# Kernel tuning notes

Hardware: AMD Instinct MI355X
Metric: run time of the kernel (lower is better)

## Reference

```python
import jax, jax.numpy as jnp
import numpy as np

# Config: 4 sparse batch items, each with 2048 active voxels (uniform-length case
# of sparse full self-attention). channels=1024, heads=16, head_dim=64.
B_SEQ, L, H, D = 4, 2048, 16, 64
C = H * D  # 1024
N = B_SEQ * L  # 8192
EPS = 1e-12  # F.normalize eps


def setup_inputs() -> dict:
    key = jax.random.key(0)
    ks = jax.random.split(key, 6)
    s = 1.0 / np.sqrt(C)
    return {
        "x": jax.random.normal(ks[0], (N, C), dtype=jnp.float32),
        "W_qkv": jax.random.normal(ks[1], (C, 3 * C), dtype=jnp.float32) * s,
        "b_qkv": jnp.zeros((3 * C,), dtype=jnp.float32),
        "gamma_q": jnp.ones((H, D), dtype=jnp.float32),
        "gamma_k": jnp.ones((H, D), dtype=jnp.float32),
        "W_out": jax.random.normal(ks[2], (C, C), dtype=jnp.float32) * s,
        "b_out": jnp.zeros((C,), dtype=jnp.float32),
    }


def _qk_rms_norm(t, gamma):
    # SparseMultiHeadRMSNorm: L2-normalize last dim, scale by gamma[h,d] * sqrt(D)
    norm = jnp.maximum(jnp.linalg.norm(t, axis=-1, keepdims=True), EPS)
    return (t / norm) * gamma * (D ** 0.5)


def reference(x, W_qkv, b_qkv, gamma_q, gamma_k, W_out, b_out):
    qkv = x @ W_qkv + b_qkv                       # [N, 3C]
    qkv = qkv.reshape(B_SEQ, L, 3, H, D)          # fused pre-reshape
    q, k, v = qkv[:, :, 0], qkv[:, :, 1], qkv[:, :, 2]  # [B,L,H,D]
    q = _qk_rms_norm(q, gamma_q)
    k = _qk_rms_norm(k, gamma_k)
    # full scaled dot-product attention within each sparse batch item
    scores = jnp.einsum('blhd,bmhd->bhlm', q, k) / (D ** 0.5)
    attn = jax.nn.softmax(scores, axis=-1)
    h = jnp.einsum('bhlm,bmhd->blhd', attn, v)    # [B,L,H,D]
    h = h.reshape(N, C)
    return h @ W_out + b_out
```

## Files before the change

kernel.cpp:

```cpp
#include <hip/hip_runtime.h>

using u16 = unsigned short;

typedef float  f32x4  __attribute__((ext_vector_type(4)));
typedef float  f32x16 __attribute__((ext_vector_type(16)));
typedef __bf16 bf16x8 __attribute__((ext_vector_type(8)));
typedef short  s16x8  __attribute__((ext_vector_type(8)));

#define DEVI __device__ __forceinline__

constexpr int TOK = 8192;
constexpr int CIN = 1024;
constexpr int C3  = 3072;
constexpr int NH  = 16;
constexpr int HD  = 64;
constexpr int SL  = 2048;
constexpr int BH  = 64;

constexpr float LOG2E = 1.4426950408889634f;

DEVI u16 f2bf(float x) {
  unsigned u = __builtin_bit_cast(unsigned, x);
  u += 0x7FFFu + ((u >> 16) & 1u);
  return (u16)(u >> 16);
}

DEVI f32x4 mfma16(s16x8 a, s16x8 b, f32x4 c) {
  return __builtin_amdgcn_mfma_f32_16x16x32_bf16(
      __builtin_bit_cast(bf16x8, a), __builtin_bit_cast(bf16x8, b), c, 0, 0, 0);
}

DEVI f32x16 mfma32(s16x8 a, s16x8 b, f32x16 c) {
  return __builtin_amdgcn_mfma_f32_32x32x16_bf16(
      __builtin_bit_cast(bf16x8, a), __builtin_bit_cast(bf16x8, b), c, 0, 0, 0);
}

DEVI void gload_lds16(const void* g, void* l) {
  __builtin_amdgcn_global_load_lds(
      (const __attribute__((address_space(1))) unsigned int*)g,
      (__attribute__((address_space(3))) unsigned int*)l, 16, 0, 0);
}

DEVI unsigned cvtpk(float lo, float hi) {
  unsigned r;
  asm("v_cvt_pk_bf16_f32 %0, %1, %2" : "=v"(r) : "v"(lo), "v"(hi));
  return r;
}

DEVI void plswap(unsigned& a, unsigned& b) {
  asm("v_permlane32_swap_b32 %0, %1" : "+v"(a), "+v"(b));
}

__global__ __launch_bounds__(256) void k_cvt_x(const float* __restrict__ x,
                                               u16* __restrict__ xb) {
  const int total = TOK * CIN / 4;
  for (int i = blockIdx.x * 256 + threadIdx.x; i < total; i += gridDim.x * 256) {
    float4 v = ((const float4*)x)[i];
    ushort4 o;
    o.x = f2bf(v.x); o.y = f2bf(v.y); o.z = f2bf(v.z); o.w = f2bf(v.w);
    ((ushort4*)xb)[i] = o;
  }
}

__global__ __launch_bounds__(256) void k_transpose(const float* __restrict__ in,
                                                   u16* __restrict__ out,
                                                   int R, int C) {
  __shared__ u16 t[64][72];
  int rt = R >> 6;
  int tr = (blockIdx.x % rt) << 6;
  int tc = (blockIdx.x / rt) << 6;
  int tid = threadIdx.x;
#pragma unroll
  for (int k2 = 0; k2 < 16; k2++) {
    int idx = k2 * 256 + tid;
    int r = idx >> 6, c = idx & 63;
    t[r][c] = f2bf(in[(size_t)(tr + r) * C + tc + c]);
  }
  __syncthreads();
#pragma unroll
  for (int k2 = 0; k2 < 16; k2++) {
    int idx = k2 * 256 + tid;
    int r = idx >> 6, c = idx & 63;
    out[(size_t)(tc + r) * R + tr + c] = t[c][r];
  }
}

__global__ __launch_bounds__(256) void k_bound(const float* __restrict__ gq,
                                               const float* __restrict__ gk,
                                               float* __restrict__ bnd) {
  const int tid = threadIdx.x;
  const int h = tid >> 4, s = tid & 15;
  float mv = 0.f;
#pragma unroll
  for (int j = 0; j < 4; j++) {
    int d = s * 4 + j;
    mv = fmaxf(mv, fabsf(gq[h * 64 + d] * gk[h * 64 + d]));
  }
  mv = fmaxf(mv, __shfl_xor(mv, 1));
  mv = fmaxf(mv, __shfl_xor(mv, 2));
  mv = fmaxf(mv, __shfl_xor(mv, 4));
  mv = fmaxf(mv, __shfl_xor(mv, 8));
  if (s == 0) bnd[h] = 8.0f * LOG2E * mv;
}

#define STAGE6(BUF, KT)                                                  \
  { char* Ld = L + (BUF) * 49152;                                        \
    const size_t ko = (size_t)(KT) * 128;                                \
    gload_lds16(Ab + ko,          Ld + wb);                              \
    gload_lds16(Ab + ko + 131072, Ld + 8192 + wb);                       \
    gload_lds16(Ab + ko + 262144, Ld + 16384 + wb);                      \
    gload_lds16(Ab + ko + 393216, Ld + 24576 + wb);                      \
    gload_lds16(Bb + ko,          Ld + 32768 + wb);                      \
    gload_lds16(Bb + ko + 131072, Ld + 40960 + wb); }

#define KBODY(KT, DOSTAGE, VMSTR)                                        \
  {                                                                      \
    if (DOSTAGE) STAGE6(((KT) + 2) % 3, (KT) + 2)                        \
    asm volatile("s_waitcnt " VMSTR ::: "memory");                       \
    __builtin_amdgcn_s_barrier();                                        \
    const char* Lb = L + ((KT) % 3) * 49152;                             \
    s16x8 af[4][2], bfr[4][2];                                           \
    _Pragma("unroll")                                                    \
    for (int mf = 0; mf < 4; mf++) {                                     \
      af[mf][0] = *(const s16x8*)(Lb + aoff + mf * 2048 + cx0);          \
      af[mf][1] = *(const s16x8*)(Lb + aoff + mf * 2048 + (cx0 ^ 64));   \
    }                                                                    \
    _Pragma("unroll")                                                    \
    for (int nf = 0; nf < 4; nf++) {                                     \
      bfr[nf][0] = *(const s16x8*)(Lb + boff + nf * 2048 + cx0);         \
      bfr[nf][1] = *(const s16x8*)(Lb + boff + nf * 2048 + (cx0 ^ 64));  \
    }                                                                    \
    __builtin_amdgcn_s_setprio(1);                                       \
    _Pragma("unroll")                                                    \
    for (int ks = 0; ks < 2; ks++)                                       \
      _Pragma("unroll")                                                  \
      for (int mf = 0; mf < 4; mf++)                                     \
        _Pragma("unroll")                                                \
        for (int nf = 0; nf < 4; nf++)                                   \
          acc[mf][nf] = mfma16(af[mf][ks], bfr[nf][ks], acc[mf][nf]);    \
    __builtin_amdgcn_s_setprio(0);                                       \
    __builtin_amdgcn_s_barrier();                                        \
  }

DEVI void gemm_mainloop(const char* Ab, const char* Bb, char* L,
                        int wb, int aoff, int boff, int cx0,
                        f32x4 (&acc)[4][4]) {
  STAGE6(0, 0)
  STAGE6(1, 1)
#pragma unroll
  for (int kt = 0; kt < 14; ++kt) KBODY(kt, 1, "vmcnt(12)")
  KBODY(14, 0, "vmcnt(6)")
  KBODY(15, 0, "vmcnt(0)")
}

__global__ __launch_bounds__(512, 2) void k_gemm_qkv(
    const u16* __restrict__ A, const u16* __restrict__ Bt,
    const float* __restrict__ bias, const float* __restrict__ gq,
    const float* __restrict__ gk,
    u16* __restrict__ Qn, u16* __restrict__ Kn, u16* __restrict__ Vt) {
  __shared__ __align__(16) char Lsh[3][49152];
  int bid = blockIdx.x;
  bid = (bid & 7) * 96 + (bid >> 3);
  const int bm = (bid / 24) * 256, bn = (bid % 24) * 128;
  const int tid = threadIdx.x, lane = tid & 63, w = tid >> 6;
  const int l15 = lane & 15, g = lane >> 4;
  const int wr4 = w >> 1, wc2 = w & 1;

  const int rA  = tid >> 3;
  const int scb = ((tid & 7) << 4) ^ ((rA & 7) << 4);
  const char* Ab = (const char*)A + (size_t)(bm + rA) * 2048 + scb;
  const char* Bb = (const char*)Bt + (size_t)(bn + rA) * 2048 + scb;
  const int wb   = w << 10;
  const int aoff = (wr4 * 64 + l15) * 128;
  const int boff = 32768 + (wc2 * 64 + l15) * 128;
  const int cx0  = (g ^ (l15 & 7)) << 4;

  f32x4 acc[4][4];
#pragma unroll
  for (int i = 0; i < 4; i++)
#pragma unroll
    for (int j = 0; j < 4; j++) acc[i][j] = f32x4{0.f, 0.f, 0.f, 0.f};

  gemm_mainloop(Ab, Bb, (char*)Lsh, wb, aoff, boff, cx0, acc);

  const int c0 = bn + wc2 * 64;
  const int sec = c0 >> 10;
  const int head = (c0 & 1023) >> 6;
  float bv[4], gv[4];
#pragma unroll
  for (int nf = 0; nf < 4; nf++) {
    bv[nf] = bias[c0 + nf * 16 + l15];
    gv[nf] = 1.f;
    if (sec == 0) gv[nf] = gq[head * 64 + nf * 16 + l15];
    if (sec == 1) gv[nf] = gk[head * 64 + nf * 16 + l15];
  }
#pragma unroll
  for (int mf = 0; mf < 4; mf++) {
#pragma unroll
    for (int nf = 0; nf < 4; nf++)
#pragma unroll
      for (int r = 0; r < 4; r++) acc[mf][nf][r] += bv[nf];
    if (sec < 2) {
#pragma unroll
      for (int r = 0; r < 4; r++) {
        float ss = 0.f;
#pragma unroll
        for (int nf = 0; nf < 4; nf++) ss += acc[mf][nf][r] * acc[mf][nf][r];
        ss += __shfl_xor(ss, 1); ss += __shfl_xor(ss, 2);
        ss += __shfl_xor(ss, 4); ss += __shfl_xor(ss, 8);
        float nrm = fmaxf(sqrtf(ss), 1e-12f);
        float f = (sec == 0 ? LOG2E : 8.0f) / nrm;
#pragma unroll
        for (int nf = 0; nf < 4; nf++) acc[mf][nf][r] *= f;
      }
    }
    int rbase = bm + wr4 * 64 + mf * 16 + 4 * g;
#pragma unroll
    for (int r = 0; r < 4; r++) {
      int row = rbase + r;
      int b = row >> 11, tok = row & 2047;
      int bh = b * NH + head;
#pragma unroll
      for (int nf = 0; nf < 4; nf++) {
        int d = nf * 16 + l15;
        u16 val = f2bf(acc[mf][nf][r] * gv[nf]);
        if (sec == 0)      Qn[((size_t)bh * SL + tok) * HD + d] = val;
        else if (sec == 1) Kn[((size_t)bh * SL + tok) * HD + d] = val;
        else               Vt[((size_t)bh * HD + d) * SL + tok] = val;
      }
    }
  }
}

__global__ __launch_bounds__(512, 2) void k_gemm_out(
    const u16* __restrict__ A, const u16* __restrict__ Bt,
    const float* __restrict__ bias, float* __restrict__ out) {
  __shared__ __align__(16) char Lsh[3][49152];
  int bid = blockIdx.x;
  bid = (bid & 7) * 32 + (bid >> 3);
  const int bm = (bid / 8) * 256, bn = (bid % 8) * 128;
  const int tid = threadIdx.x, lane = tid & 63, w = tid >> 6;
  const int l15 = lane & 15, g = lane >> 4;
  const int wr4 = w >> 1, wc2 = w & 1;

  const int rA  = tid >> 3;
  const int scb = ((tid & 7) << 4) ^ ((rA & 7) << 4);
  const char* Ab = (const char*)A + (size_t)(bm + rA) * 2048 + scb;
  const char* Bb = (const char*)Bt + (size_t)(bn + rA) * 2048 + scb;
  const int wb   = w << 10;
  const int aoff = (wr4 * 64 + l15) * 128;
  const int boff = 32768 + (wc2 * 64 + l15) * 128;
  const int cx0  = (g ^ (l15 & 7)) << 4;

  f32x4 acc[4][4];
#pragma unroll
  for (int i = 0; i < 4; i++)
#pragma unroll
    for (int j = 0; j < 4; j++) acc[i][j] = f32x4{0.f, 0.f, 0.f, 0.f};

  gemm_mainloop(Ab, Bb, (char*)Lsh, wb, aoff, boff, cx0, acc);

  float bv[4];
#pragma unroll
  for (int nf = 0; nf < 4; nf++) bv[nf] = bias[bn + wc2 * 64 + nf * 16 + l15];
#pragma unroll
  for (int mf = 0; mf < 4; mf++)
#pragma unroll
    for (int r = 0; r < 4; r++) {
      int row = bm + wr4 * 64 + mf * 16 + 4 * g + r;
#pragma unroll
      for (int nf = 0; nf < 4; nf++)
        out[(size_t)row * CIN + bn + wc2 * 64 + nf * 16 + l15] =
            acc[mf][nf][r] + bv[nf];
    }
}

__global__ __launch_bounds__(512) void k_attn(const u16* __restrict__ Qn,
                                              const u16* __restrict__ Kn,
                                              const u16* __restrict__ Vt,
                                              const float* __restrict__ bnd,
                                              u16* __restrict__ hm) {
  __shared__ __align__(16) char KL[2][8192];
  __shared__ __align__(16) char VL[2][8192];
  const int bh = blockIdx.x & 63, qb = blockIdx.x >> 6;
  const int tid = threadIdx.x, w = tid >> 6, lane = tid & 63;
  const int l31 = lane & 31, h = lane >> 5;
  const int qr0 = qb * 256 + w * 32;
  const float negM = -bnd[bh & 15];

  const int sr  = tid >> 3;
  const int scb = ((tid & 7) << 4) ^ ((sr & 7) << 4);
  const char* kst = (const char*)(Kn + (size_t)bh * SL * HD) + (size_t)sr * 128 + scb;
  const char* vst = (const char*)(Vt + (size_t)bh * HD * SL) + (size_t)sr * 4096 + scb;
  char* kl0 = KL[0] + (w << 10);
  char* vl0 = VL[0] + (w << 10);
  char* kl1 = KL[1] + (w << 10);
  char* vl1 = VL[1] + (w << 10);

  const u16* Qb = Qn + ((size_t)bh * SL + qr0 + l31) * HD + 8 * h;
  s16x8 qf[4];
#pragma unroll
  for (int ks = 0; ks < 4; ks++) qf[ks] = *(const s16x8*)(Qb + ks * 16);

  const int lb = l31 * 128 + ((h << 4) ^ ((l31 & 7) << 4));

  f32x16 o0, o1;
#pragma unroll
  for (int i = 0; i < 16; i++) { o0[i] = 0.f; o1[i] = 0.f; }
  float lr = 0.f;

  gload_lds16(kst, kl0);
  gload_lds16(vst, vl0);
  __syncthreads();

  for (int it = 0; it < 32; ++it) {
    const char* KB = (it & 1) ? KL[1] : KL[0];
    const char* VB = (it & 1) ? VL[1] : VL[0];
    if (it < 31) {
      const size_t ko = (size_t)(it + 1) << 13;
      const size_t vo = (size_t)(it + 1) << 7;
      gload_lds16(kst + ko, (it & 1) ? kl0 : kl1);
      gload_lds16(vst + vo, (it & 1) ? vl0 : vl1);
    }

    f32x16 s0, s1;
#pragma unroll
    for (int i = 0; i < 16; i++) { s0[i] = negM; s1[i] = negM; }
    __builtin_amdgcn_s_setprio(1);
#pragma unroll
    for (int ks = 0; ks < 4; ks++) {
      const s16x8 ka  = *(const s16x8*)(KB + (lb ^ (ks << 5)));
      const s16x8 kb2 = *(const s16x8*)(KB + 4096 + (lb ^ (ks << 5)));
      s0 = mfma32(ka, qf[ks], s0);
      s1 = mfma32(kb2, qf[ks], s1);
    }
    __builtin_amdgcn_s_setprio(0);

#pragma unroll
    for (int i = 0; i < 16; i++) s0[i] = __builtin_amdgcn_exp2f(s0[i]);
#pragma unroll
    for (int i = 0; i < 16; i++) s1[i] = __builtin_amdgcn_exp2f(s1[i]);
    float sm8[8];
#pragma unroll
    for (int i = 0; i < 8; i++)
      sm8[i] = (s0[i] + s0[i + 8]) + (s1[i] + s1[i + 8]);
    lr += ((sm8[0] + sm8[1]) + (sm8[2] + sm8[3])) +
          ((sm8[4] + sm8[5]) + (sm8[6] + sm8[7]));

    union PBu { unsigned u[4]; s16x8 v; } pb;
#define MK_PB(SV, B)                              \
    {                                             \
      unsigned a0 = cvtpk(SV[B + 0], SV[B + 1]);  \
      unsigned c0 = cvtpk(SV[B + 4], SV[B + 5]);  \
      plswap(a0, c0);                             \
      unsigned a1 = cvtpk(SV[B + 2], SV[B + 3]);  \
      unsigned c1 = cvtpk(SV[B + 6], SV[B + 7]);  \
      plswap(a1, c1);                             \
      pb.u[0] = a0; pb.u[1] = a1; pb.u[2] = c0; pb.u[3] = c1; \
    }
#define PV_STEP(KS)                                            \
    {                                                          \
      const s16x8 va = *(const s16x8*)(VB + (lb ^ (KS << 5))); \
      const s16x8 vb = *(const s16x8*)(VB + 4096 + (lb ^ (KS << 5))); \
      __builtin_amdgcn_s_setprio(1);                           \
      o0 = mfma32(va, pb.v, o0);                               \
      o1 = mfma32(vb, pb.v, o1);                               \
      __builtin_amdgcn_s_setprio(0);                           \
    }
    MK_PB(s0, 0) PV_STEP(0)
    MK_PB(s0, 8) PV_STEP(1)
    MK_PB(s1, 0) PV_STEP(2)
    MK_PB(s1, 8) PV_STEP(3)
#undef MK_PB
#undef PV_STEP

    __syncthreads();
  }

  const float ltot = lr + __shfl_xor(lr, 32);
  const float inv = 1.f / ltot;
  const int bq = bh >> 4, hh = bh & 15;
  u16* hb = hm + ((size_t)bq * SL + qr0 + l31) * CIN + hh * HD;
#pragma unroll
  for (int rg = 0; rg < 4; rg++) {
    const int d0 = 8 * rg + 4 * h;
    unsigned lo = cvtpk(o0[4 * rg + 0] * inv, o0[4 * rg + 1] * inv);
    unsigned hi = cvtpk(o0[4 * rg + 2] * inv, o0[4 * rg + 3] * inv);
    *(unsigned long long*)(hb + d0) =
        (unsigned long long)lo | ((unsigned long long)hi << 32);
    unsigned lo1 = cvtpk(o1[4 * rg + 0] * inv, o1[4 * rg + 1] * inv);
    unsigned hi1 = cvtpk(o1[4 * rg + 2] * inv, o1[4 * rg + 3] * inv);
    *(unsigned long long*)(hb + 32 + d0) =
        (unsigned long long)lo1 | ((unsigned long long)hi1 << 32);
  }
}

extern "C" void kernel_launch(void* const* d_in, const int* in_sizes, int n_in,
                              void* d_out, int out_size, void* d_ws, size_t ws_size,
                              hipStream_t stream) {
  const float* x    = (const float*)d_in[0];
  const float* Wqkv = (const float*)d_in[1];
  const float* bqkv = (const float*)d_in[2];
  const float* gq   = (const float*)d_in[3];
  const float* gk   = (const float*)d_in[4];
  const float* Wout = (const float*)d_in[5];
  const float* bout = (const float*)d_in[6];
  float* out = (float*)d_out;

  char* ws = (char*)d_ws;
  u16* xb  = (u16*)(ws);
  u16* wqT = (u16*)(ws + 16777216);
  u16* woT = (u16*)(ws + 23068672);
  u16* Qn  = (u16*)(ws + 25165824);
  u16* Kn  = (u16*)(ws + 41943040);
  u16* Vt  = (u16*)(ws + 58720256);
  u16* hm  = (u16*)(ws + 75497472);
  float* bnd = (float*)xb;

  k_cvt_x<<<2048, 256, 0, stream>>>(x, xb);
  k_transpose<<<(1024 / 64) * (3072 / 64), 256, 0, stream>>>(Wqkv, wqT, 1024, 3072);
  k_transpose<<<(1024 / 64) * (1024 / 64), 256, 0, stream>>>(Wout, woT, 1024, 1024);
  k_gemm_qkv<<<(TOK / 256) * (C3 / 128), 512, 0, stream>>>(xb, wqT, bqkv, gq, gk, Qn, Kn, Vt);
  k_bound<<<1, 256, 0, stream>>>(gq, gk, bnd);
  k_attn<<<BH * (SL / 256), 512, 0, stream>>>(Qn, Kn, Vt, bnd, hm);
  k_gemm_out<<<(TOK / 256) * (CIN / 128), 512, 0, stream>>>(hm, woT, bout, out);
}
```

Baseline: 205.1 us.

## Enlarge QKV GEMM tile to 256x256 with interleaved double-buffered pipeline

Rewrites the QKV projection GEMM to use 256x256 output tiles per block (8 waves arranged 2x4, 8x4 MFMA fragments per wave) instead of 256x128, halving the grid. The triple-buffered mainloop is replaced by a two-buffer scheme of 64 KB each, where A/B half-tile loads for the next k-steps are interleaved between quarter-tile MFMA phases separated by barriers. The goal is higher arithmetic intensity per LDS and global byte and fewer redundant A loads. In exchange it doubles accumulator registers, uses 128 KB LDS per block (likely one block per CU), adds many barriers, and leaves 384 blocks to spread over the CUs.

```diff
diff --git a/kernel.cpp b/kernel.cpp
--- a/kernel.cpp
+++ b/kernel.cpp
@@ -101,6 +101,166 @@
   mv = fmaxf(mv, __shfl_xor(mv, 4));
   mv = fmaxf(mv, __shfl_xor(mv, 8));
   if (s == 0) bnd[h] = 8.0f * LOG2E * mv;
+}
+
+__global__ __launch_bounds__(512, 2) void k_gemm_qkv(
+    const u16* __restrict__ A, const u16* __restrict__ Bt,
+    const float* __restrict__ bias, const float* __restrict__ gq,
+    const float* __restrict__ gk,
+    u16* __restrict__ Qn, u16* __restrict__ Kn, u16* __restrict__ Vt) {
+  __shared__ __align__(16) char Lsh[2][65536];
+  char* Lb0 = (char*)Lsh;
+  int bid = blockIdx.x;
+  bid = (bid & 7) * 48 + (bid >> 3);
+  const int bm = (bid / 12) * 256, bn = (bid % 12) * 256;
+  const int tid = threadIdx.x, lane = tid & 63, w = tid >> 6;
+  const int l15 = lane & 15, g = lane >> 4;
+  const int wm = w >> 2, wn = w & 3;
+  const int wb = w << 10;
+
+  const int sw = ((tid & 7) << 4) ^ (((tid >> 3) & 7) << 4);
+  const char* srcA = (const char*)A + (size_t)(bm + (tid >> 3)) * 2048 + sw;
+  const char* srcB = (const char*)Bt + (size_t)(bn + (tid >> 3)) * 2048 + sw;
+
+  const int xr = (l15 & 7) << 4;
+  const int cb0 = (g << 4) ^ xr;
+  const int cb1 = (64 | (g << 4)) ^ xr;
+  const int aRow = (wm * 128 + l15) * 128;
+  const int bRow = 32768 + (wn * 64 + l15) * 128;
+
+  f32x4 acc[8][4];
+#pragma unroll
+  for (int i = 0; i < 8; i++)
+#pragma unroll
+    for (int j = 0; j < 4; j++) acc[i][j] = f32x4{0.f, 0.f, 0.f, 0.f};
+
+#define SGA(BUF, KT, R0) \
+  gload_lds16(srcA + (R0) * 2048 + (KT) * 128, Lb0 + (BUF) + (R0) * 128 + wb)
+#define SGB(BUF, KT, R0) \
+  gload_lds16(srcB + (R0) * 2048 + (KT) * 128, Lb0 + (BUF) + 32768 + (R0) * 128 + wb)
+#define RDA(DST, BUF, ROFF)                                                      \
+  _Pragma("unroll")                                                              \
+  for (int mf = 0; mf < 4; mf++) {                                               \
+    DST[mf][0] = *(const s16x8*)(Lb0 + (BUF) + aRow + (ROFF) + mf * 2048 + cb0); \
+    DST[mf][1] = *(const s16x8*)(Lb0 + (BUF) + aRow + (ROFF) + mf * 2048 + cb1); \
+  }
+#define RDB(N0, BUF)                                                                   \
+  _Pragma("unroll")                                                                    \
+  for (int nf = 0; nf < 2; nf++) {                                                     \
+    bf[(N0) + nf][0] = *(const s16x8*)(Lb0 + (BUF) + bRow + ((N0) + nf) * 2048 + cb0); \
+    bf[(N0) + nf][1] = *(const s16x8*)(Lb0 + (BUF) + bRow + ((N0) + nf) * 2048 + cb1); \
+  }
+#define MMQ(AFV, MB, NB)                                                       \
+  __builtin_amdgcn_s_setprio(1);                                               \
+  _Pragma("unroll")                                                            \
+  for (int ks = 0; ks < 2; ks++)                                               \
+    _Pragma("unroll")                                                          \
+    for (int mf = 0; mf < 4; mf++)                                             \
+      _Pragma("unroll")                                                        \
+      for (int nf = 0; nf < 2; nf++)                                           \
+        acc[(MB) + mf][(NB) + nf] = mfma16(AFV[mf][ks], bf[(NB) + nf][ks],     \
+                                           acc[(MB) + mf][(NB) + nf]);         \
+  __builtin_amdgcn_s_setprio(0);
+#define BAR __builtin_amdgcn_s_barrier()
+#define LGKM0 asm volatile("s_waitcnt lgkmcnt(0)" ::: "memory")
+#define VM4 asm volatile("s_waitcnt vmcnt(4)" ::: "memory")
+
+  SGA(0, 0, 0); SGA(0, 0, 64); SGA(0, 0, 128); SGA(0, 0, 192);
+  SGB(0, 0, 0); SGB(0, 0, 64); SGB(0, 0, 128); SGB(0, 0, 192);
+  SGB(65536, 1, 0); SGB(65536, 1, 64); SGB(65536, 1, 128); SGB(65536, 1, 192);
+  VM4;
+  BAR;
+
+#pragma unroll
+  for (int i = 0; i < 8; ++i) {
+    s16x8 af[4][2], bf[4][2], af2[4][2];
+    RDA(af, 0, 0) RDB(0, 0)
+    SGA(65536, 2 * i + 1, 0); SGA(65536, 2 * i + 1, 64);
+    BAR; LGKM0; MMQ(af, 0, 0) BAR;
+    RDB(2, 0)
+    SGA(65536, 2 * i + 1, 128); SGA(65536, 2 * i + 1, 192);
+    BAR; LGKM0; MMQ(af, 0, 2) BAR;
+    RDA(af2, 0, 8192)
+    if (i < 7) { SGB(0, 2 * i + 2, 0); SGB(0, 2 * i + 2, 64); }
+    BAR; LGKM0; MMQ(af2, 4, 0) BAR;
+    if (i < 7) {
+      SGB(0, 2 * i + 2, 128); SGB(0, 2 * i + 2, 192);
+      VM4;
+    } else {
+      asm volatile("s_waitcnt vmcnt(0)" ::: "memory");
+    }
+    BAR; LGKM0; MMQ(af2, 4, 2) BAR;
+    RDA(af, 65536, 0) RDB(0, 65536)
+    if (i < 7) { SGA(0, 2 * i + 2, 0); SGA(0, 2 * i + 2, 64); }
+    BAR; LGKM0; MMQ(af, 0, 0) BAR;
+    RDB(2, 65536)
+    if (i < 7) { SGA(0, 2 * i + 2, 128); SGA(0, 2 * i + 2, 192); }
+    BAR; LGKM0; MMQ(af, 0, 2) BAR;
+    RDA(af2, 65536, 8192)
+    if (i < 7) { SGB(65536, 2 * i + 3, 0); SGB(65536, 2 * i + 3, 64); }
+    BAR; LGKM0; MMQ(af2, 4, 0) BAR;
+    if (i < 7) {
+      SGB(65536, 2 * i + 3, 128); SGB(65536, 2 * i + 3, 192);
+      VM4;
+    }
+    BAR; LGKM0; MMQ(af2, 4, 2) BAR;
+  }
+#undef SGA
+#undef SGB
+#undef RDA
+#undef RDB
+#undef MMQ
+#undef BAR
+#undef LGKM0
+#undef VM4
+
+  const int c0 = bn + wn * 64;
+  const int sec = c0 >> 10;
+  const int head = (c0 & 1023) >> 6;
+  float bv[4], gv[4];
+#pragma unroll
+  for (int nf = 0; nf < 4; nf++) {
+    bv[nf] = bias[c0 + nf * 16 + l15];
+    gv[nf] = 1.f;
+    if (sec == 0) gv[nf] = gq[head * 64 + nf * 16 + l15];
+    if (sec == 1) gv[nf] = gk[head * 64 + nf * 16 + l15];
+  }
+#pragma unroll
+  for (int mf = 0; mf < 8; mf++) {
+#pragma unroll
+    for (int nf = 0; nf < 4; nf++)
+#pragma unroll
+      for (int r = 0; r < 4; r++) acc[mf][nf][r] += bv[nf];
+    if (sec < 2) {
+#pragma unroll
+      for (int r = 0; r < 4; r++) {
+        float ss = 0.f;
+#pragma unroll
+        for (int nf = 0; nf < 4; nf++) ss += acc[mf][nf][r] * acc[mf][nf][r];
+        ss += __shfl_xor(ss, 1); ss += __shfl_xor(ss, 2);
+        ss += __shfl_xor(ss, 4); ss += __shfl_xor(ss, 8);
+        float nrm = fmaxf(sqrtf(ss), 1e-12f);
+        float f = (sec == 0 ? LOG2E : 8.0f) / nrm;
+#pragma unroll
+        for (int nf = 0; nf < 4; nf++) acc[mf][nf][r] *= f;
+      }
+    }
+    int rbase = bm + wm * 128 + mf * 16 + 4 * g;
+#pragma unroll
+    for (int r = 0; r < 4; r++) {
+      int row = rbase + r;
+      int b = row >> 11, tok = row & 2047;
+      int bh = b * NH + head;
+#pragma unroll
+      for (int nf = 0; nf < 4; nf++) {
+        int d = nf * 16 + l15;
+        u16 val = f2bf(acc[mf][nf][r] * gv[nf]);
+        if (sec == 0)      Qn[((size_t)bh * SL + tok) * HD + d] = val;
+        else if (sec == 1) Kn[((size_t)bh * SL + tok) * HD + d] = val;
+        else               Vt[((size_t)bh * HD + d) * SL + tok] = val;
+      }
+    }
+  }
 }
 
 #define STAGE6(BUF, KT)                                                  \
@@ -153,85 +313,6 @@
   KBODY(15, 0, "vmcnt(0)")
 }
 
-__global__ __launch_bounds__(512, 2) void k_gemm_qkv(
-    const u16* __restrict__ A, const u16* __restrict__ Bt,
-    const float* __restrict__ bias, const float* __restrict__ gq,
-    const float* __restrict__ gk,
-    u16* __restrict__ Qn, u16* __restrict__ Kn, u16* __restrict__ Vt) {
-  __shared__ __align__(16) char Lsh[3][49152];
-  int bid = blockIdx.x;
-  bid = (bid & 7) * 96 + (bid >> 3);
-  const int bm = (bid / 24) * 256, bn = (bid % 24) * 128;
-  const int tid = threadIdx.x, lane = tid & 63, w = tid >> 6;
-  const int l15 = lane & 15, g = lane >> 4;
-  const int wr4 = w >> 1, wc2 = w & 1;
-
-  const int rA  = tid >> 3;
-  const int scb = ((tid & 7) << 4) ^ ((rA & 7) << 4);
-  const char* Ab = (const char*)A + (size_t)(bm + rA) * 2048 + scb;
-  const char* Bb = (const char*)Bt + (size_t)(bn + rA) * 2048 + scb;
-  const int wb   = w << 10;
-  const int aoff = (wr4 * 64 + l15) * 128;
-  const int boff = 32768 + (wc2 * 64 + l15) * 128;
-  const int cx0  = (g ^ (l15 & 7)) << 4;
-
-  f32x4 acc[4][4];
-#pragma unroll
-  for (int i = 0; i < 4; i++)
-#pragma unroll
-    for (int j = 0; j < 4; j++) acc[i][j] = f32x4{0.f, 0.f, 0.f, 0.f};
-
-  gemm_mainloop(Ab, Bb, (char*)Lsh, wb, aoff, boff, cx0, acc);
-
-  const int c0 = bn + wc2 * 64;
-  const int sec = c0 >> 10;
-  const int head = (c0 & 1023) >> 6;
-  float bv[4], gv[4];
-#pragma unroll
-  for (int nf = 0; nf < 4; nf++) {
-    bv[nf] = bias[c0 + nf * 16 + l15];
-    gv[nf] = 1.f;
-    if (sec == 0) gv[nf] = gq[head * 64 + nf * 16 + l15];
-    if (sec == 1) gv[nf] = gk[head * 64 + nf * 16 + l15];
-  }
-#pragma unroll
-  for (int mf = 0; mf < 4; mf++) {
-#pragma unroll
-    for (int nf = 0; nf < 4; nf++)
-#pragma unroll
-      for (int r = 0; r < 4; r++) acc[mf][nf][r] += bv[nf];
-    if (sec < 2) {
-#pragma unroll
-      for (int r = 0; r < 4; r++) {
-        float ss = 0.f;
-#pragma unroll
-        for (int nf = 0; nf < 4; nf++) ss += acc[mf][nf][r] * acc[mf][nf][r];
-        ss += __shfl_xor(ss, 1); ss += __shfl_xor(ss, 2);
-        ss += __shfl_xor(ss, 4); ss += __shfl_xor(ss, 8);
-        float nrm = fmaxf(sqrtf(ss), 1e-12f);
-        float f = (sec == 0 ? LOG2E : 8.0f) / nrm;
-#pragma unroll
-        for (int nf = 0; nf < 4; nf++) acc[mf][nf][r] *= f;
-      }
-    }
-    int rbase = bm + wr4 * 64 + mf * 16 + 4 * g;
-#pragma unroll
-    for (int r = 0; r < 4; r++) {
-      int row = rbase + r;
-      int b = row >> 11, tok = row & 2047;
-      int bh = b * NH + head;
-#pragma unroll
-      for (int nf = 0; nf < 4; nf++) {
-        int d = nf * 16 + l15;
-        u16 val = f2bf(acc[mf][nf][r] * gv[nf]);
-        if (sec == 0)      Qn[((size_t)bh * SL + tok) * HD + d] = val;
-        else if (sec == 1) Kn[((size_t)bh * SL + tok) * HD + d] = val;
-        else               Vt[((size_t)bh * HD + d) * SL + tok] = val;
-      }
-    }
-  }
-}
-
 __global__ __launch_bounds__(512, 2) void k_gemm_out(
     const u16* __restrict__ A, const u16* __restrict__ Bt,
     const float* __restrict__ bias, float* __restrict__ out) {
@@ -420,7 +501,7 @@
   k_cvt_x<<<2048, 256, 0, stream>>>(x, xb);
   k_transpose<<<(1024 / 64) * (3072 / 64), 256, 0, stream>>>(Wqkv, wqT, 1024, 3072);
   k_transpose<<<(1024 / 64) * (1024 / 64), 256, 0, stream>>>(Wout, woT, 1024, 1024);
-  k_gemm_qkv<<<(TOK / 256) * (C3 / 128), 512, 0, stream>>>(xb, wqT, bqkv, gq, gk, Qn, Kn, Vt);
+  k_gemm_qkv<<<(TOK / 256) * (C3 / 256), 512, 0, stream>>>(xb, wqT, bqkv, gq, gk, Qn, Kn, Vt);
   k_bound<<<1, 256, 0, stream>>>(gq, gk, bnd);
   k_attn<<<BH * (SL / 256), 512, 0, stream>>>(Qn, Kn, Vt, bnd, hm);
   k_gemm_out<<<(TOK / 256) * (CIN / 128), 512, 0, stream>>>(hm, woT, bout, out);
```

After: 210.1 us. +2.4%, slower.

## Shrink GEMM tiles to 128x128 with 32-wide K steps and 256 threads

Applied to the files above, without the earlier changes.

Both projection GEMMs move from 256x128 tiles with 512 threads and a K step of 64 to 128x128 tiles with 256 threads and a K step of 32, using a three-slot 16KB LDS ring. The grid doubles and occupancy rises to 3 blocks per CU, aiming for better load balance and latency hiding across the CUs. The XOR swizzle on the LDS layout is dropped, so ds_read bank conflicts may appear. Smaller tiles also reduce operand reuse, and the loop now runs twice as many iterations, each with its own barriers.

```diff
diff --git a/kernel.cpp b/kernel.cpp
--- a/kernel.cpp
+++ b/kernel.cpp
@@ -103,77 +103,64 @@
   if (s == 0) bnd[h] = 8.0f * LOG2E * mv;
 }
 
-#define STAGE6(BUF, KT)                                                  \
-  { char* Ld = L + (BUF) * 49152;                                        \
-    const size_t ko = (size_t)(KT) * 128;                                \
-    gload_lds16(Ab + ko,          Ld + wb);                              \
-    gload_lds16(Ab + ko + 131072, Ld + 8192 + wb);                       \
-    gload_lds16(Ab + ko + 262144, Ld + 16384 + wb);                      \
-    gload_lds16(Ab + ko + 393216, Ld + 24576 + wb);                      \
-    gload_lds16(Bb + ko,          Ld + 32768 + wb);                      \
-    gload_lds16(Bb + ko + 131072, Ld + 40960 + wb); }
-
-#define KBODY(KT, DOSTAGE, VMSTR)                                        \
+#define STAGE4(SLOT, KT)                                                 \
+  { char* Ld = L + (SLOT) * 16384;                                       \
+    const size_t ko = (size_t)(KT) * 64;              \
+    gload_lds16(Ag + ko,          Ld + wq);                              \
+    gload_lds16(Ag + ko + 131072, Ld + 4096 + wq);                       \
+    gload_lds16(Bg + ko,          Ld + 8192 + wq);                       \
+    gload_lds16(Bg + ko + 131072, Ld + 12288 + wq); }
+
+#define KBODY32(KT, DOSTAGE, VMSTR)                                      \
   {                                                                      \
-    if (DOSTAGE) STAGE6(((KT) + 2) % 3, (KT) + 2)                        \
+    if (DOSTAGE) STAGE4(((KT) + 2) % 3, (KT) + 2)                        \
     asm volatile("s_waitcnt " VMSTR ::: "memory");                       \
     __builtin_amdgcn_s_barrier();                                        \
-    const char* Lb = L + ((KT) % 3) * 49152;                             \
-    s16x8 af[4][2], bfr[4][2];                                           \
+    const char* Lb = L + ((KT) % 3) * 16384;                             \
+    s16x8 af[4], bfr[4];                                                 \
     _Pragma("unroll")                                                    \
-    for (int mf = 0; mf < 4; mf++) {                                     \
-      af[mf][0] = *(const s16x8*)(Lb + aoff + mf * 2048 + cx0);          \
-      af[mf][1] = *(const s16x8*)(Lb + aoff + mf * 2048 + (cx0 ^ 64));   \
-    }                                                                    \
+    for (int mf = 0; mf < 4; mf++)                                       \
+      af[mf] = *(const s16x8*)(Lb + (wr + mf * 16 + l15) * 64 + g * 16); \
     _Pragma("unroll")                                                    \
-    for (int nf = 0; nf < 4; nf++) {                                     \
-      bfr[nf][0] = *(const s16x8*)(Lb + boff + nf * 2048 + cx0);         \
-      bfr[nf][1] = *(const s16x8*)(Lb + boff + nf * 2048 + (cx0 ^ 64));  \
-    }                                                                    \
+    for (int nf = 0; nf < 4; nf++)                                       \
+      bfr[nf] = *(const s16x8*)(Lb + 8192 + (wc + nf * 16 + l15) * 64 + g * 16); \
     __builtin_amdgcn_s_setprio(1);                                       \
     _Pragma("unroll")                                                    \
-    for (int ks = 0; ks < 2; ks++)                                       \
+    for (int mf = 0; mf < 4; mf++)                                       \
       _Pragma("unroll")                                                  \
-      for (int mf = 0; mf < 4; mf++)                                     \
-        _Pragma("unroll")                                                \
-        for (int nf = 0; nf < 4; nf++)                                   \
-          acc[mf][nf] = mfma16(af[mf][ks], bfr[nf][ks], acc[mf][nf]);    \
+      for (int nf = 0; nf < 4; nf++)                                     \
+        acc[mf][nf] = mfma16(af[mf], bfr[nf], acc[mf][nf]);              \
     __builtin_amdgcn_s_setprio(0);                                       \
     __builtin_amdgcn_s_barrier();                                        \
   }
 
-DEVI void gemm_mainloop(const char* Ab, const char* Bb, char* L,
-                        int wb, int aoff, int boff, int cx0,
-                        f32x4 (&acc)[4][4]) {
-  STAGE6(0, 0)
-  STAGE6(1, 1)
-#pragma unroll
-  for (int kt = 0; kt < 14; ++kt) KBODY(kt, 1, "vmcnt(12)")
-  KBODY(14, 0, "vmcnt(6)")
-  KBODY(15, 0, "vmcnt(0)")
-}
-
-__global__ __launch_bounds__(512, 2) void k_gemm_qkv(
+DEVI void gemm_mainloop(const char* Ag, const char* Bg, char* L, int wq,
+                        int wr, int wc, int l15, int g, f32x4 (&acc)[4][4]) {
+  STAGE4(0, 0)
+  STAGE4(1, 1)
+#pragma unroll
+  for (int kt = 0; kt < 30; ++kt) KBODY32(kt, 1, "vmcnt(8)")
+  KBODY32(30, 0, "vmcnt(4)")
+  KBODY32(31, 0, "vmcnt(0)")
+}
+
+__global__ __launch_bounds__(256, 3) void k_gemm_qkv(
     const u16* __restrict__ A, const u16* __restrict__ Bt,
     const float* __restrict__ bias, const float* __restrict__ gq,
     const float* __restrict__ gk,
     u16* __restrict__ Qn, u16* __restrict__ Kn, u16* __restrict__ Vt) {
-  __shared__ __align__(16) char Lsh[3][49152];
+  __shared__ __align__(16) char Lsh[3][16384];
   int bid = blockIdx.x;
-  bid = (bid & 7) * 96 + (bid >> 3);
-  const int bm = (bid / 24) * 256, bn = (bid % 24) * 128;
+  bid = (bid & 7) * 192 + (bid >> 3);
+  const int bm = (bid / 24) * 128, bn = (bid % 24) * 128;
   const int tid = threadIdx.x, lane = tid & 63, w = tid >> 6;
   const int l15 = lane & 15, g = lane >> 4;
-  const int wr4 = w >> 1, wc2 = w & 1;
-
-  const int rA  = tid >> 3;
-  const int scb = ((tid & 7) << 4) ^ ((rA & 7) << 4);
-  const char* Ab = (const char*)A + (size_t)(bm + rA) * 2048 + scb;
-  const char* Bb = (const char*)Bt + (size_t)(bn + rA) * 2048 + scb;
-  const int wb   = w << 10;
-  const int aoff = (wr4 * 64 + l15) * 128;
-  const int boff = 32768 + (wc2 * 64 + l15) * 128;
-  const int cx0  = (g ^ (l15 & 7)) << 4;
+  const int wr = (w >> 1) * 64, wc = (w & 1) * 64;
+
+  const int srow = tid >> 2, scol = (tid & 3) * 16;
+  const char* Ag = (const char*)A + (size_t)(bm + srow) * 2048 + scol;
+  const char* Bg = (const char*)Bt + (size_t)(bn + srow) * 2048 + scol;
+  const int wq = w << 10;
 
   f32x4 acc[4][4];
 #pragma unroll
@@ -181,9 +168,9 @@
 #pragma unroll
     for (int j = 0; j < 4; j++) acc[i][j] = f32x4{0.f, 0.f, 0.f, 0.f};
 
-  gemm_mainloop(Ab, Bb, (char*)Lsh, wb, aoff, boff, cx0, acc);
-
-  const int c0 = bn + wc2 * 64;
+  gemm_mainloop(Ag, Bg, (char*)Lsh, wq, wr, wc, l15, g, acc);
+
+  const int c0 = bn + wc;
   const int sec = c0 >> 10;
   const int head = (c0 & 1023) >> 6;
   float bv[4], gv[4];
@@ -214,7 +201,7 @@
         for (int nf = 0; nf < 4; nf++) acc[mf][nf][r] *= f;
       }
     }
-    int rbase = bm + wr4 * 64 + mf * 16 + 4 * g;
+    int rbase = bm + wr + mf * 16 + 4 * g;
 #pragma unroll
     for (int r = 0; r < 4; r++) {
       int row = rbase + r;
@@ -232,25 +219,21 @@
   }
 }
 
-__global__ __launch_bounds__(512, 2) void k_gemm_out(
+__global__ __launch_bounds__(256, 3) void k_gemm_out(
     const u16* __restrict__ A, const u16* __restrict__ Bt,
     const float* __restrict__ bias, float* __restrict__ out) {
-  __shared__ __align__(16) char Lsh[3][49152];
+  __shared__ __align__(16) char Lsh[3][16384];
   int bid = blockIdx.x;
-  bid = (bid & 7) * 32 + (bid >> 3);
-  const int bm = (bid / 8) * 256, bn = (bid % 8) * 128;
+  bid = (bid & 7) * 64 + (bid >> 3);
+  const int bm = (bid / 8) * 128, bn = (bid % 8) * 128;
   const int tid = threadIdx.x, lane = tid & 63, w = tid >> 6;
   const int l15 = lane & 15, g = lane >> 4;
-  const int wr4 = w >> 1, wc2 = w & 1;
-
-  const int rA  = tid >> 3;
-  const int scb = ((tid & 7) << 4) ^ ((rA & 7) << 4);
-  const char* Ab = (const char*)A + (size_t)(bm + rA) * 2048 + scb;
-  const char* Bb = (const char*)Bt + (size_t)(bn + rA) * 2048 + scb;
-  const int wb   = w << 10;
-  const int aoff = (wr4 * 64 + l15) * 128;
-  const int boff = 32768 + (wc2 * 64 + l15) * 128;
-  const int cx0  = (g ^ (l15 & 7)) << 4;
+  const int wr = (w >> 1) * 64, wc = (w & 1) * 64;
+
+  const int srow = tid >> 2, scol = (tid & 3) * 16;
+  const char* Ag = (const char*)A + (size_t)(bm + srow) * 2048 + scol;
+  const char* Bg = (const char*)Bt + (size_t)(bn + srow) * 2048 + scol;
+  const int wq = w << 10;
 
   f32x4 acc[4][4];
 #pragma unroll
@@ -258,20 +241,19 @@
 #pragma unroll
     for (int j = 0; j < 4; j++) acc[i][j] = f32x4{0.f, 0.f, 0.f, 0.f};
 
-  gemm_mainloop(Ab, Bb, (char*)Lsh, wb, aoff, boff, cx0, acc);
+  gemm_mainloop(Ag, Bg, (char*)Lsh, wq, wr, wc, l15, g, acc);
 
   float bv[4];
 #pragma unroll
-  for (int nf = 0; nf < 4; nf++) bv[nf] = bias[bn + wc2 * 64 + nf * 16 + l15];
+  for (int nf = 0; nf < 4; nf++) bv[nf] = bias[bn + wc + nf * 16 + l15];
 #pragma unroll
   for (int mf = 0; mf < 4; mf++)
 #pragma unroll
     for (int r = 0; r < 4; r++) {
-      int row = bm + wr4 * 64 + mf * 16 + 4 * g + r;
+      int row = bm + wr + mf * 16 + 4 * g + r;
 #pragma unroll
       for (int nf = 0; nf < 4; nf++)
-        out[(size_t)row * CIN + bn + wc2 * 64 + nf * 16 + l15] =
-            acc[mf][nf][r] + bv[nf];
+        out[(size_t)row * CIN + bn + wc + nf * 16 + l15] = acc[mf][nf][r] + bv[nf];
     }
 }
 
@@ -420,8 +402,8 @@
   k_cvt_x<<<2048, 256, 0, stream>>>(x, xb);
   k_transpose<<<(1024 / 64) * (3072 / 64), 256, 0, stream>>>(Wqkv, wqT, 1024, 3072);
   k_transpose<<<(1024 / 64) * (1024 / 64), 256, 0, stream>>>(Wout, woT, 1024, 1024);
-  k_gemm_qkv<<<(TOK / 256) * (C3 / 128), 512, 0, stream>>>(xb, wqT, bqkv, gq, gk, Qn, Kn, Vt);
+  k_gemm_qkv<<<(TOK / 128) * (C3 / 128), 256, 0, stream>>>(xb, wqT, bqkv, gq, gk, Qn, Kn, Vt);
   k_bound<<<1, 256, 0, stream>>>(gq, gk, bnd);
   k_attn<<<BH * (SL / 256), 512, 0, stream>>>(Qn, Kn, Vt, bnd, hm);
-  k_gemm_out<<<(TOK / 256) * (CIN / 128), 512, 0, stream>>>(hm, woT, bout, out);
-}
+  k_gemm_out<<<(TOK / 128) * (CIN / 128), 256, 0, stream>>>(hm, woT, bout, out);
+}
```

Result: no change. 208.8 us (+1.8%).
